# Kernel tuning notes

Hardware: AMD Instinct MI355X
Metric: run time of the kernel (lower is better)

## Reference

```python
import jax, jax.numpy as jnp
import numpy as np

N_NODES = 50000
N_EDGES = 500000
H_DIM = 128
BN_EPS = 1e-5


def setup_inputs() -> dict:
    key = jax.random.key(0)
    k1, k2, k3, k4 = jax.random.split(key, 4)
    ent_emb = jax.random.normal(k1, (N_NODES, H_DIM), dtype=jnp.float32)
    neigh_w = jax.random.normal(k2, (H_DIM, H_DIM), dtype=jnp.float32) * 0.05
    gamma = jnp.ones((H_DIM,), dtype=jnp.float32)
    beta = jnp.zeros((H_DIM,), dtype=jnp.float32)
    src = jax.random.randint(k3, (N_EDGES,), 0, N_NODES, dtype=jnp.int32)
    dst = jax.random.randint(k4, (N_EDGES,), 0, N_NODES, dtype=jnp.int32)
    return {"ent_emb": ent_emb, "neigh_w": neigh_w, "gamma": gamma,
            "beta": beta, "src": src, "dst": dst}


def reference(ent_emb, neigh_w, gamma, beta, src, dst):
    # u_dot_v: per-edge dot product of src and dst node embeddings -> [E]
    e_src = ent_emb[src]                      # [E, D] gather
    scores = jnp.sum(e_src * ent_emb[dst], axis=-1)  # [E]

    # edge_softmax: softmax over incoming edges of each destination node
    seg_max = jax.ops.segment_max(scores, dst, num_segments=N_NODES)
    seg_max = jnp.where(jnp.isfinite(seg_max), seg_max, 0.0)  # empty nodes
    ex = jnp.exp(scores - seg_max[dst])
    denom = jax.ops.segment_sum(ex, dst, num_segments=N_NODES)
    norm = ex / denom[dst]                    # [E]

    # u_mul_e + sum: weighted scatter-sum of src embeddings into dst nodes
    neigh = jax.ops.segment_sum(e_src * norm[:, None], dst,
                                num_segments=N_NODES)  # [N, D]

    # linear + BatchNorm1d (training mode, batch stats) + tanh
    h = neigh @ neigh_w
    mu = jnp.mean(h, axis=0)
    var = jnp.var(h, axis=0)                  # biased, matches torch BN
    h = (h - mu) * jax.lax.rsqrt(var + BN_EPS) * gamma + beta
    return jnp.tanh(h)
```

## Files before the change

kernel.cpp:

```cpp
#include <hip/hip_runtime.h>
#include <hip/hip_bf16.h>
#include <math.h>

#define N_NODES 50000
#define N_EDGES 500000
#define H_DIM   128
#define BN_EPS  1e-5f
#define GEMM_GRID ((N_NODES + 31) / 32)
#define SCAN_NBLK ((N_NODES + 255) / 256)
#define RED_NBLK  64

typedef __attribute__((ext_vector_type(8))) short short8;
typedef __attribute__((ext_vector_type(4))) float floatx4;

__device__ __forceinline__ ushort f2bf(float x)
{
    unsigned u = __float_as_uint(x);
    unsigned r = (u + 0x7FFFu + ((u >> 16) & 1u)) >> 16;
    return (ushort)r;
}

__global__ __launch_bounds__(256) void hist_cvt_kernel(
    const int* __restrict__ dst, int* __restrict__ deg,
    const float* __restrict__ W, ushort* __restrict__ wt)
{
    int e = blockIdx.x * blockDim.x + threadIdx.x;
    if (e < N_EDGES) atomicAdd(&deg[dst[e]], 1);
    if (e < H_DIM * H_DIM) {
        int k = e >> 7, c = e & 127;
        wt[c * 128 + k] = f2bf(W[e]);
    }
}

__global__ __launch_bounds__(256) void scan_partial_kernel(
    const int* __restrict__ deg, int* __restrict__ blocksum)
{
    __shared__ int red[256];
    int t = threadIdx.x;
    int i = blockIdx.x * 256 + t;
    red[t] = (i < N_NODES) ? deg[i] : 0;
    __syncthreads();
    #pragma unroll
    for (int off = 128; off; off >>= 1) {
        if (t < off) red[t] += red[t + off];
        __syncthreads();
    }
    if (t == 0) blocksum[blockIdx.x] = red[0];
}

__global__ __launch_bounds__(256) void scan_final_kernel(
    const int* __restrict__ deg, const int* __restrict__ blocksum,
    int* __restrict__ rowptr, int* __restrict__ cursor)
{
    __shared__ int bs[256];
    __shared__ int s[256];
    int t = threadIdx.x;

    bs[t] = (t < SCAN_NBLK) ? blocksum[t] : 0;
    __syncthreads();
    for (int off = 1; off < 256; off <<= 1) {
        int v = (t >= off) ? bs[t - off] : 0;
        __syncthreads();
        bs[t] += v;
        __syncthreads();
    }
    int blockoff = (blockIdx.x == 0) ? 0 : bs[blockIdx.x - 1];

    int i = blockIdx.x * 256 + t;
    int v = (i < N_NODES) ? deg[i] : 0;
    s[t] = v;
    __syncthreads();
    for (int off = 1; off < 256; off <<= 1) {
        int u = (t >= off) ? s[t - off] : 0;
        __syncthreads();
        s[t] += u;
        __syncthreads();
    }
    int excl = s[t] - v + blockoff;
    if (i < N_NODES) {
        rowptr[i] = excl;
        cursor[i] = excl;
        if (i == N_NODES - 1) rowptr[N_NODES] = excl + v;
    }
}

__global__ __launch_bounds__(256) void csr_scatter_kernel(
    const int* __restrict__ src, const int* __restrict__ dst,
    int* __restrict__ cursor, int* __restrict__ csr_src)
{
    int e = blockIdx.x * blockDim.x + threadIdx.x;
    if (e >= N_EDGES) return;
    int pos = atomicAdd(&cursor[dst[e]], 1);
    csr_src[pos] = src[e];
}

__global__ __launch_bounds__(256, 3) void fused_agg_gemm_kernel(
    const float* __restrict__ emb,
    const int* __restrict__ rowptr,
    const int* __restrict__ csr_src,
    const ushort* __restrict__ wt,
    float* __restrict__ h,
    float* __restrict__ partial)
{
    __shared__ ushort A_s[32 * 128];
    __shared__ ushort W_s[128 * 128];
    __shared__ float  red_s[128 * 9];
    __shared__ float  red_q[128 * 9];

    int t  = threadIdx.x;
    int r0 = blockIdx.x * 32;

    for (int g = t; g < 128 * 16; g += 256) {
        int c = g >> 4, gk = g & 15;
        short8 v = *(const short8*)(wt + (size_t)c * 128 + gk * 8);
        int idx = c * 128 + ((gk * 8) ^ ((c & 7) << 3));
        *(short8*)&W_s[idx] = v;
    }

    int grp  = t >> 5;
    int lane = t & 31;

    for (int ri = 0; ri < 4; ++ri) {
        int row  = ri * 8 + grp;
        int node = r0 + row;
        float4 o = {0.f, 0.f, 0.f, 0.f};

        if (node < N_NODES) {
            int beg = rowptr[node];
            int end = rowptr[node + 1];
            const float4 b = *((const float4*)(emb + (size_t)node * H_DIM) + lane);

            float m = -INFINITY;
            float denom = 0.f;
            float4 acc = {0.f, 0.f, 0.f, 0.f};

            int e = beg;
            for (; e + 8 <= end; e += 8) {
                float4 a[8];
                float  p[8];
                #pragma unroll
                for (int u = 0; u < 8; ++u) {
                    int s = csr_src[e + u];
                    a[u] = *((const float4*)(emb + (size_t)s * H_DIM) + lane);
                }
                #pragma unroll
                for (int u = 0; u < 8; ++u)
                    p[u] = a[u].x * b.x + a[u].y * b.y + a[u].z * b.z + a[u].w * b.w;
                #pragma unroll
                for (int off = 16; off; off >>= 1) {
                    #pragma unroll
                    for (int u = 0; u < 8; ++u)
                        p[u] += __shfl_xor(p[u], off);
                }
                float mn = m;
                #pragma unroll
                for (int u = 0; u < 8; ++u) mn = fmaxf(mn, p[u]);
                float corr = __expf(m - mn);
                float w[8];
                #pragma unroll
                for (int u = 0; u < 8; ++u) w[u] = __expf(p[u] - mn);
                float wsum = 0.f;
                #pragma unroll
                for (int u = 0; u < 8; ++u) wsum += w[u];
                denom = denom * corr + wsum;
                float sx = 0.f, sy = 0.f, sz = 0.f, sw = 0.f;
                #pragma unroll
                for (int u = 0; u < 8; ++u) {
                    sx += a[u].x * w[u];
                    sy += a[u].y * w[u];
                    sz += a[u].z * w[u];
                    sw += a[u].w * w[u];
                }
                acc.x = acc.x * corr + sx;
                acc.y = acc.y * corr + sy;
                acc.z = acc.z * corr + sz;
                acc.w = acc.w * corr + sw;
                m = mn;
            }
            if (e + 4 <= end) {
                float4 a[4];
                float  p[4];
                #pragma unroll
                for (int u = 0; u < 4; ++u) {
                    int s = csr_src[e + u];
                    a[u] = *((const float4*)(emb + (size_t)s * H_DIM) + lane);
                }
                #pragma unroll
                for (int u = 0; u < 4; ++u)
                    p[u] = a[u].x * b.x + a[u].y * b.y + a[u].z * b.z + a[u].w * b.w;
                #pragma unroll
                for (int off = 16; off; off >>= 1) {
                    #pragma unroll
                    for (int u = 0; u < 4; ++u)
                        p[u] += __shfl_xor(p[u], off);
                }
                float mn = fmaxf(fmaxf(fmaxf(p[0], p[1]), fmaxf(p[2], p[3])), m);
                float corr = __expf(m - mn);
                float w[4];
                #pragma unroll
                for (int u = 0; u < 4; ++u) w[u] = __expf(p[u] - mn);
                denom = denom * corr + w[0] + w[1] + w[2] + w[3];
                acc.x = acc.x * corr + a[0].x*w[0] + a[1].x*w[1] + a[2].x*w[2] + a[3].x*w[3];
                acc.y = acc.y * corr + a[0].y*w[0] + a[1].y*w[1] + a[2].y*w[2] + a[3].y*w[3];
                acc.z = acc.z * corr + a[0].z*w[0] + a[1].z*w[1] + a[2].z*w[2] + a[3].z*w[3];
                acc.w = acc.w * corr + a[0].w*w[0] + a[1].w*w[1] + a[2].w*w[2] + a[3].w*w[3];
                m = mn;
                e += 4;
            }
            for (; e < end; ++e) {
                int s = csr_src[e];
                float4 a = *((const float4*)(emb + (size_t)s * H_DIM) + lane);
                float p = a.x * b.x + a.y * b.y + a.z * b.z + a.w * b.w;
                #pragma unroll
                for (int off = 16; off; off >>= 1)
                    p += __shfl_xor(p, off);
                float mn   = fmaxf(m, p);
                float corr = __expf(m - mn);
                float w    = __expf(p - mn);
                denom = denom * corr + w;
                acc.x = acc.x * corr + a.x * w;
                acc.y = acc.y * corr + a.y * w;
                acc.z = acc.z * corr + a.z * w;
                acc.w = acc.w * corr + a.w * w;
                m = mn;
            }

            float inv = (end > beg) ? (1.0f / denom) : 0.f;
            o.x = acc.x * inv; o.y = acc.y * inv;
            o.z = acc.z * inv; o.w = acc.w * inv;
        }

        unsigned lo = (unsigned)f2bf(o.x) | ((unsigned)f2bf(o.y) << 16);
        unsigned hi = (unsigned)f2bf(o.z) | ((unsigned)f2bf(o.w) << 16);
        int col = (lane * 4) ^ ((row & 7) << 3);
        uint2 pk; pk.x = lo; pk.y = hi;
        *(uint2*)&A_s[row * 128 + col] = pk;
    }
    __syncthreads();

    int w    = t >> 6;
    int lane64 = t & 63;
    int rbase = (w >> 1) * 16;
    int c0    = (w & 1) * 64;
    int l15   = lane64 & 15;
    int kgrp  = lane64 >> 4;
    int arow  = rbase + l15;
    int k0l   = kgrp * 8;

    floatx4 acc4[4] = {{0.f,0.f,0.f,0.f},{0.f,0.f,0.f,0.f},
                       {0.f,0.f,0.f,0.f},{0.f,0.f,0.f,0.f}};

    #pragma unroll
    for (int ks = 0; ks < 4; ++ks) {
        int k0 = ks * 32 + k0l;
        short8 af = *(const short8*)&A_s[arow * 128 + (k0 ^ ((arow & 7) << 3))];
        #pragma unroll
        for (int ct = 0; ct < 4; ++ct) {
            int col = c0 + ct * 16 + l15;
            short8 bf = *(const short8*)&W_s[col * 128 + (k0 ^ ((col & 7) << 3))];
            acc4[ct] = __builtin_amdgcn_mfma_f32_16x16x32_bf16(af, bf, acc4[ct], 0, 0, 0);
        }
    }

    int contrib = (w >> 1) * 4 + kgrp;
    #pragma unroll
    for (int ct = 0; ct < 4; ++ct) {
        int col = c0 + ct * 16 + l15;
        float ps = 0.f, pq = 0.f;
        #pragma unroll
        for (int reg = 0; reg < 4; ++reg) {
            float v = acc4[ct][reg];
            int gr = r0 + rbase + kgrp * 4 + reg;
            if (gr < N_NODES) h[(size_t)gr * H_DIM + col] = v;
            ps += v;
            pq += v * v;
        }
        red_s[col * 9 + contrib] = ps;
        red_q[col * 9 + contrib] = pq;
    }
    __syncthreads();

    float s = 0.f;
    if (t < 128) {
        #pragma unroll
        for (int q = 0; q < 8; ++q) s += red_s[t * 9 + q];
    } else if (t < 256) {
        #pragma unroll
        for (int q = 0; q < 8; ++q) s += red_q[(t - 128) * 9 + q];
    }
    partial[(size_t)blockIdx.x * 256 + t] = s;
}

__global__ __launch_bounds__(256) void reduce_partials_kernel(
    const float* __restrict__ partial, float* __restrict__ partial2)
{
    int t = threadIdx.x;
    int g = blockIdx.x;
    float s = 0.f;
    for (int b = g; b < GEMM_GRID; b += RED_NBLK)
        s += partial[(size_t)b * 256 + t];
    partial2[(size_t)g * 256 + t] = s;
}

__global__ __launch_bounds__(1024) void bn_stats_kernel(
    const float* __restrict__ partial2,
    const float* __restrict__ gamma,
    const float* __restrict__ beta,
    float* __restrict__ scale,
    float* __restrict__ shift)
{
    __shared__ float tot[4][256];
    __shared__ float tot2[256];
    int v = threadIdx.x & 255;
    int q = threadIdx.x >> 8;
    float s = 0.f;
    for (int b = q; b < RED_NBLK; b += 4)
        s += partial2[(size_t)b * 256 + v];
    tot[q][v] = s;
    __syncthreads();
    if (threadIdx.x < 256)
        tot2[v] = tot[0][v] + tot[1][v] + tot[2][v] + tot[3][v];
    __syncthreads();
    if (threadIdx.x < 128) {
        int c = threadIdx.x;
        float cs = tot2[c];
        float cq = tot2[c + 128];
        const float invN = 1.0f / (float)N_NODES;
        float mu  = cs * invN;
        float var = cq * invN - mu * mu;
        float sc  = gamma[c] * rsqrtf(var + BN_EPS);
        scale[c] = sc;
        shift[c] = beta[c] - mu * sc;
    }
}

__global__ __launch_bounds__(256) void bn_tanh_kernel(
    float* __restrict__ h,
    const float* __restrict__ scale,
    const float* __restrict__ shift)
{
    size_t i = (size_t)blockIdx.x * blockDim.x + threadIdx.x;
    size_t idx4 = i * 4;
    if (idx4 >= (size_t)N_NODES * H_DIM) return;
    int c = (int)(idx4 & (H_DIM - 1));
    float4 v = *(float4*)(h + idx4);
    v.x = tanhf(v.x * scale[c + 0] + shift[c + 0]);
    v.y = tanhf(v.y * scale[c + 1] + shift[c + 1]);
    v.z = tanhf(v.z * scale[c + 2] + shift[c + 2]);
    v.w = tanhf(v.w * scale[c + 3] + shift[c + 3]);
    *(float4*)(h + idx4) = v;
}

extern "C" void kernel_launch(void* const* d_in, const int* in_sizes, int n_in,
                              void* d_out, int out_size, void* d_ws, size_t ws_size,
                              hipStream_t stream)
{
    const float* ent_emb = (const float*)d_in[0];
    const float* neigh_w = (const float*)d_in[1];
    const float* gamma   = (const float*)d_in[2];
    const float* beta    = (const float*)d_in[3];
    const int*   src     = (const int*)d_in[4];
    const int*   dst     = (const int*)d_in[5];
    float* out = (float*)d_out;

    int*    deg      = (int*)d_ws;
    int*    rowptr   = deg + N_NODES;
    int*    cursor   = rowptr + N_NODES + 1;
    int*    csr_src  = cursor + N_NODES;
    int*    blocksum = csr_src + N_EDGES;
    float*  partial  = (float*)(blocksum + SCAN_NBLK);
    float*  partial2 = partial + (size_t)GEMM_GRID * 256;
    ushort* wt       = (ushort*)(partial2 + (size_t)RED_NBLK * 256);
    float*  scale    = (float*)(wt + H_DIM * H_DIM);
    float*  shift    = scale + H_DIM;

    hipMemsetAsync(deg, 0, N_NODES * sizeof(int), stream);

    hist_cvt_kernel<<<(N_EDGES + 255) / 256, 256, 0, stream>>>(dst, deg, neigh_w, wt);
    scan_partial_kernel<<<SCAN_NBLK, 256, 0, stream>>>(deg, blocksum);
    scan_final_kernel<<<SCAN_NBLK, 256, 0, stream>>>(deg, blocksum, rowptr, cursor);
    csr_scatter_kernel<<<(N_EDGES + 255) / 256, 256, 0, stream>>>(src, dst, cursor, csr_src);

    fused_agg_gemm_kernel<<<GEMM_GRID, 256, 0, stream>>>(
        ent_emb, rowptr, csr_src, wt, out, partial);

    reduce_partials_kernel<<<RED_NBLK, 256, 0, stream>>>(partial, partial2);
    bn_stats_kernel<<<1, 1024, 0, stream>>>(partial2, gamma, beta, scale, shift);
    {
        size_t total4 = (size_t)N_NODES * H_DIM / 4;
        int blocks = (int)((total4 + 255) / 256);
        bn_tanh_kernel<<<blocks, 256, 0, stream>>>(out, scale, shift);
    }
}
```

Measured before the change: 164.6 us.

## Drop shared W tile, read weights from global, and raise occupancy

Removes the 32 KB shared-memory copy of the bf16 weight matrix. The MFMA B-fragments are now loaded directly from global memory, where the data is expected to stay in cache. The 8-wide edge unroll is dropped in favour of a 4-wide loop to cut register use, and the launch-bounds occupancy hint is raised from 3 to 8 blocks. Together these aim at more resident waves to hide the latency of the gather-bound aggregation, at the cost of global loads in the GEMM phase and less memory-level parallelism per thread.

Result: faster. 157.3 us (-4.4%).

```diff
diff --git a/kernel.cpp b/kernel.cpp
--- a/kernel.cpp
+++ b/kernel.cpp
@@ -94,7 +94,7 @@
     csr_src[pos] = src[e];
 }
 
-__global__ __launch_bounds__(256, 3) void fused_agg_gemm_kernel(
+__global__ __launch_bounds__(256, 8) void fused_agg_gemm_kernel(
     const float* __restrict__ emb,
     const int* __restrict__ rowptr,
     const int* __restrict__ csr_src,
@@ -103,19 +103,11 @@
     float* __restrict__ partial)
 {
     __shared__ ushort A_s[32 * 128];
-    __shared__ ushort W_s[128 * 128];
     __shared__ float  red_s[128 * 9];
     __shared__ float  red_q[128 * 9];
 
     int t  = threadIdx.x;
     int r0 = blockIdx.x * 32;
-
-    for (int g = t; g < 128 * 16; g += 256) {
-        int c = g >> 4, gk = g & 15;
-        short8 v = *(const short8*)(wt + (size_t)c * 128 + gk * 8);
-        int idx = c * 128 + ((gk * 8) ^ ((c & 7) << 3));
-        *(short8*)&W_s[idx] = v;
-    }
 
     int grp  = t >> 5;
     int lane = t & 31;
@@ -135,49 +127,7 @@
             float4 acc = {0.f, 0.f, 0.f, 0.f};
 
             int e = beg;
-            for (; e + 8 <= end; e += 8) {
-                float4 a[8];
-                float  p[8];
-                #pragma unroll
-                for (int u = 0; u < 8; ++u) {
-                    int s = csr_src[e + u];
-                    a[u] = *((const float4*)(emb + (size_t)s * H_DIM) + lane);
-                }
-                #pragma unroll
-                for (int u = 0; u < 8; ++u)
-                    p[u] = a[u].x * b.x + a[u].y * b.y + a[u].z * b.z + a[u].w * b.w;
-                #pragma unroll
-                for (int off = 16; off; off >>= 1) {
-                    #pragma unroll
-                    for (int u = 0; u < 8; ++u)
-                        p[u] += __shfl_xor(p[u], off);
-                }
-                float mn = m;
-                #pragma unroll
-                for (int u = 0; u < 8; ++u) mn = fmaxf(mn, p[u]);
-                float corr = __expf(m - mn);
-                float w[8];
-                #pragma unroll
-                for (int u = 0; u < 8; ++u) w[u] = __expf(p[u] - mn);
-                float wsum = 0.f;
-                #pragma unroll
-                for (int u = 0; u < 8; ++u) wsum += w[u];
-                denom = denom * corr + wsum;
-                float sx = 0.f, sy = 0.f, sz = 0.f, sw = 0.f;
-                #pragma unroll
-                for (int u = 0; u < 8; ++u) {
-                    sx += a[u].x * w[u];
-                    sy += a[u].y * w[u];
-                    sz += a[u].z * w[u];
-                    sw += a[u].w * w[u];
-                }
-                acc.x = acc.x * corr + sx;
-                acc.y = acc.y * corr + sy;
-                acc.z = acc.z * corr + sz;
-                acc.w = acc.w * corr + sw;
-                m = mn;
-            }
-            if (e + 4 <= end) {
+            for (; e + 4 <= end; e += 4) {
                 float4 a[4];
                 float  p[4];
                 #pragma unroll
@@ -205,7 +155,6 @@
                 acc.z = acc.z * corr + a[0].z*w[0] + a[1].z*w[1] + a[2].z*w[2] + a[3].z*w[3];
                 acc.w = acc.w * corr + a[0].w*w[0] + a[1].w*w[1] + a[2].w*w[2] + a[3].w*w[3];
                 m = mn;
-                e += 4;
             }
             for (; e < end; ++e) {
                 int s = csr_src[e];
@@ -238,14 +187,14 @@
     }
     __syncthreads();
 
-    int w    = t >> 6;
+    int w      = t >> 6;
     int lane64 = t & 63;
-    int rbase = (w >> 1) * 16;
-    int c0    = (w & 1) * 64;
-    int l15   = lane64 & 15;
-    int kgrp  = lane64 >> 4;
-    int arow  = rbase + l15;
-    int k0l   = kgrp * 8;
+    int rbase  = (w >> 1) * 16;
+    int c0     = (w & 1) * 64;
+    int l15    = lane64 & 15;
+    int kgrp   = lane64 >> 4;
+    int arow   = rbase + l15;
+    int k0l    = kgrp * 8;
 
     floatx4 acc4[4] = {{0.f,0.f,0.f,0.f},{0.f,0.f,0.f,0.f},
                        {0.f,0.f,0.f,0.f},{0.f,0.f,0.f,0.f}};
@@ -257,7 +206,7 @@
         #pragma unroll
         for (int ct = 0; ct < 4; ++ct) {
             int col = c0 + ct * 16 + l15;
-            short8 bf = *(const short8*)&W_s[col * 128 + (k0 ^ ((col & 7) << 3))];
+            short8 bf = *(const short8*)(wt + (size_t)col * 128 + k0);
             acc4[ct] = __builtin_amdgcn_mfma_f32_16x16x32_bf16(af, bf, acc4[ct], 0, 0, 0);
         }
     }
```
